# Kernel tuning notes

Hardware: AMD Instinct MI355X
Metric: run time of the kernel (lower is better)

## Reference

```python
import jax, jax.numpy as jnp
import numpy as np

BSZ, SEQ, D_IN = 256, 512, 1
STATE, D_OUT, KX = 512, 512, 5


def setup_inputs() -> dict:
    key = jax.random.key(0)
    k1, k2, k3, k4, k5, k6 = jax.random.split(key, 6)
    inputs = jax.random.normal(k1, (BSZ, SEQ, D_IN), dtype=jnp.float32)
    # diagonal transition, kept stable in (0, 0.99)
    A = jax.random.uniform(k2, (STATE,), dtype=jnp.float32, minval=0.0, maxval=0.99)
    B = jax.random.normal(k3, (D_IN, STATE), dtype=jnp.float32) * 0.05
    C = jax.random.normal(k4, (STATE, D_OUT), dtype=jnp.float32) * 0.05
    M = jax.random.normal(k5, (D_OUT, D_IN, KX), dtype=jnp.float32) * 0.05
    h0 = jax.random.normal(k6, (STATE,), dtype=jnp.float32)
    return {"inputs": inputs, "A": A, "B": B, "C": C, "M": M, "h0": h0}


def reference(inputs, A, B, C, M, h0):
    """LDS forward: h_t = A*h_{t-1} + x_t @ B; y_t = h_t @ C + sum_i M[:,:,i] x_{t-1-i}.
    inputs: [B, T, 1] -> out: [B, T, D_OUT]
    """
    bsz, T, _ = inputs.shape
    h_init = jnp.broadcast_to(h0, (bsz, h0.shape[0]))  # reset_state: h = h0 per batch row

    xs = jnp.swapaxes(inputs, 0, 1)  # [T, B, 1]

    def step(h, x_t):
        h = h * A + x_t @ B  # [B, STATE]
        return h, h

    _, hs = jax.lax.scan(step, h_init, xs)  # hs: [T, B, STATE]
    lds_out = jnp.einsum('tbs,so->bto', hs, C)  # [B, T, D_OUT]

    # AR ring buffer: at step t it holds x_{t-1}..x_{t-kx} (zeros before t=0),
    # tap i multiplies M[:,:,i]. With d_in==1 this is a delayed causal conv.
    x = inputs[:, :, 0]  # [B, T]
    kx = M.shape[-1]
    shifted = jnp.stack(
        [jnp.pad(x, ((0, 0), (i + 1, 0)))[:, :T] for i in range(kx)], axis=-1
    )  # [B, T, kx]; entry i is x_{t-1-i}
    ar_out = jnp.einsum('btk,ok->bto', shifted, M[:, 0, :])  # [B, T, D_OUT]

    return lds_out + ar_out
```

## Files before the change

kernel.cpp:

```cpp
#include <hip/hip_runtime.h>


typedef __attribute__((ext_vector_type(8))) short short8v;
typedef __attribute__((ext_vector_type(4))) float float4v;

#define NB 16
#define SIG(e) ((e) + ((e) >> 3))
#define AWI(j) ((((j) % 6) + 6) % 6)

static __device__ __forceinline__ unsigned short f2bf(float f) {
    union { float f; unsigned int u; } x; x.f = f;
    unsigned int r = x.u + 0x7fffu + ((x.u >> 16) & 1u);
    return (unsigned short)(r >> 16);
}

__global__ __launch_bounds__(256) void k_prep(const float* __restrict__ A,
                                              const float* __restrict__ B,
                                              const float* __restrict__ h0,
                                              const float* __restrict__ C,
                                              const float* __restrict__ M,
                                              const float* __restrict__ x,
                                              unsigned short* __restrict__ KT,
                                              float* __restrict__ G,
                                              short8v* __restrict__ XS) {
    __shared__ float PBL[512][4];
    __shared__ float PHL[512][4];
    __shared__ float red[4][64][8];
    __shared__ unsigned short xs[512];
    const int tid = threadIdx.x;

    if (blockIdx.x < 1024) {
        const int d0 = (blockIdx.x & 127) * 4;
        const int oc = blockIdx.x >> 7;

        #pragma unroll
        for (int q = 0; q < 2; ++q) {
            int ss = tid + q * 256;
            float a = A[ss];
            float r = 1.0f, base = a;
            #pragma unroll
            for (int bit = 0; bit < 9; ++bit) {
                if (d0 & (1 << bit)) r *= base;
                base *= base;
            }
            float bs = B[ss], hs = h0[ss];
            #pragma unroll
            for (int j = 0; j < 4; ++j) {
                PBL[ss][j] = r * bs;
                PHL[ss][j] = r * a * hs;
                r *= a;
            }
        }
        __syncthreads();

        const int lane = tid & 63;
        const int sc   = tid >> 6;
        const int o    = oc * 64 + lane;
        float kt[4] = {0.f, 0.f, 0.f, 0.f};
        float gg[4] = {0.f, 0.f, 0.f, 0.f};
        for (int si = 0; si < 128; si += 8) {
            float c8[8];
            #pragma unroll
            for (int u = 0; u < 8; ++u)
                c8[u] = C[(sc * 128 + si + u) * 512 + o];
            #pragma unroll
            for (int u = 0; u < 8; ++u) {
                int s = sc * 128 + si + u;
                #pragma unroll
                for (int j = 0; j < 4; ++j) {
                    kt[j] = fmaf(PBL[s][j], c8[u], kt[j]);
                    gg[j] = fmaf(PHL[s][j], c8[u], gg[j]);
                }
            }
        }
        #pragma unroll
        for (int j = 0; j < 4; ++j) {
            red[sc][lane][j]     = kt[j];
            red[sc][lane][j + 4] = gg[j];
        }
        __syncthreads();
        if (sc == 0) {
            #pragma unroll
            for (int j = 0; j < 4; ++j) {
                float v  = red[0][lane][j] + red[1][lane][j]
                         + red[2][lane][j] + red[3][lane][j];
                float gv = red[0][lane][j+4] + red[1][lane][j+4]
                         + red[2][lane][j+4] + red[3][lane][j+4];
                int d = d0 + j;
                if (d >= 1 && d <= 5) v += M[o * 5 + (d - 1)];
                KT[o * 512 + d] = f2bf(v);
                G[d * 512 + o]  = gv;
            }
        }
    } else {
        const int b = blockIdx.x - 1024;
        #pragma unroll
        for (int q = 0; q < 2; ++q) {
            int i = tid * 2 + q;
            xs[i] = f2bf(x[b * 512 + 511 - i]);
        }
        __syncthreads();
        short8v* dst = XS + (size_t)b * 1216;
        for (int s2 = tid; s2 < 1216; s2 += 256) {
            if (s2 % 9 == 8 || s2 > 1150) dst[s2] = (short8v)(short)0;
        }
        #pragma unroll
        for (int q = 0; q < 4; ++q) {
            int e = tid * 4 + q;
            short8v v;
            #pragma unroll
            for (int jj = 0; jj < 8; ++jj) {
                int i = e + jj;
                v[jj] = (i < 512) ? (short)xs[i] : (short)0;
            }
            dst[SIG(e)] = v;
        }
    }
}

__global__ __launch_bounds__(256, 2) void k_main(const short8v* __restrict__ XS,
                                                 const unsigned short* __restrict__ KT,
                                                 const float* __restrict__ G,
                                                 float* __restrict__ out) {
    __shared__ short8v xbuf[2][1216];

    const int bo0 = blockIdx.x * 32;
    const int bt0 = blockIdx.y * 256;
    const int b0  = blockIdx.z * NB;
    const int tid = threadIdx.x;
    const int lane = tid & 63;
    const int wv   = tid >> 6;
    const int t0w  = bt0 + wv * 64;
    const int lrow = lane & 15;
    const int g    = lane >> 4;

    {
        const short8v* src = XS + (size_t)b0 * 1216;
        for (int c = wv; c < 19; c += 4)
            __builtin_amdgcn_global_load_lds(
                (const __attribute__((address_space(1))) void*)(src + c * 64 + lane),
                (__attribute__((address_space(3))) void*)(&xbuf[0][c * 64]),
                16, 0, 0);
    }

    short8v bfr[2][16];
    #pragma unroll
    for (int ni = 0; ni < 2; ++ni) {
        const unsigned short* bp = KT + (bo0 + ni * 16 + lrow) * 512 + g * 8;
        #pragma unroll
        for (int ks = 0; ks < 16; ++ks)
            bfr[ni][ks] = *(const short8v*)(bp + ks * 32);
    }

    float4v gacc[4][2];
    #pragma unroll
    for (int mi = 0; mi < 4; ++mi)
        #pragma unroll
        for (int ni = 0; ni < 2; ++ni)
            gacc[mi][ni] = *(const float4v*)(G + (t0w + mi * 16 + lrow) * 512
                                               + bo0 + ni * 16 + g * 4);

    asm volatile("s_waitcnt vmcnt(0)" ::: "memory");
    __builtin_amdgcn_s_barrier();

    const int E0 = 511 - t0w - lrow + g * 8;

    int p = 0;
    for (int bi = 0; bi < NB; ++bi) {
        const int b = b0 + bi;

        if (bi + 1 < NB) {
            const short8v* src = XS + (size_t)(b + 1) * 1216;
            short8v* dstb = xbuf[p ^ 1];
            for (int c = wv; c < 19; c += 4)
                __builtin_amdgcn_global_load_lds(
                    (const __attribute__((address_space(1))) void*)(src + c * 64 + lane),
                    (__attribute__((address_space(3))) void*)(dstb + c * 64),
                    16, 0, 0);
        }

        const short8v* xo = xbuf[p];

        float4v acc[4][2];
        #pragma unroll
        for (int mi = 0; mi < 4; ++mi)
            #pragma unroll
            for (int ni = 0; ni < 2; ++ni)
                acc[mi][ni] = (float4v)(0.0f);

        short8v aw[6];
        #pragma unroll
        for (int j = -3; j <= 0; ++j)
            aw[AWI(j)] = xo[SIG(E0 + 16 * j)];

        __builtin_amdgcn_s_setprio(1);
        #pragma unroll
        for (int ks = 0; ks < 16; ++ks) {
            acc[3][0] = __builtin_amdgcn_mfma_f32_16x16x32_bf16(
                bfr[0][ks], aw[AWI(2 * ks - 3)], acc[3][0], 0, 0, 0);
            acc[3][1] = __builtin_amdgcn_mfma_f32_16x16x32_bf16(
                bfr[1][ks], aw[AWI(2 * ks - 3)], acc[3][1], 0, 0, 0);
            acc[2][0] = __builtin_amdgcn_mfma_f32_16x16x32_bf16(
                bfr[0][ks], aw[AWI(2 * ks - 2)], acc[2][0], 0, 0, 0);
            acc[2][1] = __builtin_amdgcn_mfma_f32_16x16x32_bf16(
                bfr[1][ks], aw[AWI(2 * ks - 2)], acc[2][1], 0, 0, 0);
            if (ks < 15) {
                aw[AWI(2 * ks + 1)] = xo[SIG(E0 + 16 * (2 * ks + 1))];
                aw[AWI(2 * ks + 2)] = xo[SIG(E0 + 16 * (2 * ks + 2))];
            }
            acc[1][0] = __builtin_amdgcn_mfma_f32_16x16x32_bf16(
                bfr[0][ks], aw[AWI(2 * ks - 1)], acc[1][0], 0, 0, 0);
            acc[1][1] = __builtin_amdgcn_mfma_f32_16x16x32_bf16(
                bfr[1][ks], aw[AWI(2 * ks - 1)], acc[1][1], 0, 0, 0);
            acc[0][0] = __builtin_amdgcn_mfma_f32_16x16x32_bf16(
                bfr[0][ks], aw[AWI(2 * ks)], acc[0][0], 0, 0, 0);
            acc[0][1] = __builtin_amdgcn_mfma_f32_16x16x32_bf16(
                bfr[1][ks], aw[AWI(2 * ks)], acc[0][1], 0, 0, 0);
        }
        __builtin_amdgcn_s_setprio(0);

        float* op = out + (size_t)b * 262144;
        #pragma unroll
        for (int mi = 0; mi < 4; ++mi) {
            const int t = t0w + mi * 16 + lrow;
            float* rp = op + t * 512 + bo0 + g * 4;
            *(float4v*)(rp)      = acc[mi][0] + gacc[mi][0];
            *(float4v*)(rp + 16) = acc[mi][1] + gacc[mi][1];
        }

        if (bi + 1 < NB) {
            asm volatile("s_waitcnt vmcnt(8)" ::: "memory");
            __builtin_amdgcn_s_barrier();
            p ^= 1;
        }
    }
}

extern "C" void kernel_launch(void* const* d_in, const int* in_sizes, int n_in,
                              void* d_out, int out_size, void* d_ws, size_t ws_size,
                              hipStream_t stream) {
    const float* x  = (const float*)d_in[0];
    const float* A  = (const float*)d_in[1];
    const float* B  = (const float*)d_in[2];
    const float* C  = (const float*)d_in[3];
    const float* M  = (const float*)d_in[4];
    const float* h0 = (const float*)d_in[5];
    float* out = (float*)d_out;

    char* ws = (char*)d_ws;
    unsigned short* KT = (unsigned short*)ws;
    float*          G  = (float*)(ws + (1u << 19));
    short8v*        XS = (short8v*)(ws + (1u << 19) + (1u << 20));

    k_prep<<<1280, 256, 0, stream>>>(A, B, h0, C, M, x, KT, G, XS);
    k_main<<<dim3(16, 2, 16), 256, 0, stream>>>(XS, KT, G, out);
}
```

Before: 87.09 us.

## Load sliding input windows directly from global memory instead of staging in LDS

Removes the double-buffered LDS staging of the per-batch Toeplitz input octets, along with the padded swizzle layout and its barriers. Each lane now reads its A-operand windows straight from a dense global buffer through registers, with an 8-deep register ring and prefetch of the next batch's window during the epilogue. The G bias is folded in as the initial accumulator value. This drops LDS traffic and block-wide synchronization, but relies on cache hits for the redundant global reads and exposes global load latency inside the MFMA loop.

```diff
diff --git a/kernel.cpp b/kernel.cpp
--- a/kernel.cpp
+++ b/kernel.cpp
@@ -5,8 +5,6 @@
 typedef __attribute__((ext_vector_type(4))) float float4v;
 
 #define NB 16
-#define SIG(e) ((e) + ((e) >> 3))
-#define AWI(j) ((((j) % 6) + 6) % 6)
 
 static __device__ __forceinline__ unsigned short f2bf(float f) {
     union { float f; unsigned int u; } x; x.f = f;
@@ -22,7 +20,7 @@
                                               const float* __restrict__ x,
                                               unsigned short* __restrict__ KT,
                                               float* __restrict__ G,
-                                              short8v* __restrict__ XS) {
+                                              short8v* __restrict__ XOCT) {
     __shared__ float PBL[512][4];
     __shared__ float PHL[512][4];
     __shared__ float red[4][64][8];
@@ -100,10 +98,7 @@
             xs[i] = f2bf(x[b * 512 + 511 - i]);
         }
         __syncthreads();
-        short8v* dst = XS + (size_t)b * 1216;
-        for (int s2 = tid; s2 < 1216; s2 += 256) {
-            if (s2 % 9 == 8 || s2 > 1150) dst[s2] = (short8v)(short)0;
-        }
+        short8v* dst = XOCT + (size_t)b * 1024;
         #pragma unroll
         for (int q = 0; q < 4; ++q) {
             int e = tid * 4 + q;
@@ -113,36 +108,25 @@
                 int i = e + jj;
                 v[jj] = (i < 512) ? (short)xs[i] : (short)0;
             }
-            dst[SIG(e)] = v;
+            dst[e] = v;
         }
     }
 }
 
-__global__ __launch_bounds__(256, 2) void k_main(const short8v* __restrict__ XS,
+__global__ __launch_bounds__(256, 2) void k_main(const short8v* __restrict__ XOCT,
                                                  const unsigned short* __restrict__ KT,
                                                  const float* __restrict__ G,
                                                  float* __restrict__ out) {
-    __shared__ short8v xbuf[2][1216];
-
     const int bo0 = blockIdx.x * 32;
     const int bt0 = blockIdx.y * 256;
     const int b0  = blockIdx.z * NB;
-    const int tid = threadIdx.x;
+    const int tid  = threadIdx.x;
     const int lane = tid & 63;
     const int wv   = tid >> 6;
     const int t0w  = bt0 + wv * 64;
     const int lrow = lane & 15;
     const int g    = lane >> 4;
 
-    {
-        const short8v* src = XS + (size_t)b0 * 1216;
-        for (int c = wv; c < 19; c += 4)
-            __builtin_amdgcn_global_load_lds(
-                (const __attribute__((address_space(1))) void*)(src + c * 64 + lane),
-                (__attribute__((address_space(3))) void*)(&xbuf[0][c * 64]),
-                16, 0, 0);
-    }
-
     short8v bfr[2][16];
     #pragma unroll
     for (int ni = 0; ni < 2; ++ni) {
@@ -151,7 +135,6 @@
         for (int ks = 0; ks < 16; ++ks)
             bfr[ni][ks] = *(const short8v*)(bp + ks * 32);
     }
-
     float4v gacc[4][2];
     #pragma unroll
     for (int mi = 0; mi < 4; ++mi)
@@ -160,78 +143,62 @@
             gacc[mi][ni] = *(const float4v*)(G + (t0w + mi * 16 + lrow) * 512
                                                + bo0 + ni * 16 + g * 4);
 
-    asm volatile("s_waitcnt vmcnt(0)" ::: "memory");
-    __builtin_amdgcn_s_barrier();
-
-    const int E0 = 511 - t0w - lrow + g * 8;
-
-    int p = 0;
+    const int E0 = 511 - t0w - lrow + 8 * g;
+    const short8v* xw = XOCT + (size_t)b0 * 1024 + E0;
+
+    short8v aw[8];
+    #pragma unroll
+    for (int j = -3; j <= 4; ++j)
+        aw[j & 7] = xw[16 * j];
+
     for (int bi = 0; bi < NB; ++bi) {
-        const int b = b0 + bi;
-
-        if (bi + 1 < NB) {
-            const short8v* src = XS + (size_t)(b + 1) * 1216;
-            short8v* dstb = xbuf[p ^ 1];
-            for (int c = wv; c < 19; c += 4)
-                __builtin_amdgcn_global_load_lds(
-                    (const __attribute__((address_space(1))) void*)(src + c * 64 + lane),
-                    (__attribute__((address_space(3))) void*)(dstb + c * 64),
-                    16, 0, 0);
-        }
-
-        const short8v* xo = xbuf[p];
-
         float4v acc[4][2];
         #pragma unroll
         for (int mi = 0; mi < 4; ++mi)
             #pragma unroll
             for (int ni = 0; ni < 2; ++ni)
-                acc[mi][ni] = (float4v)(0.0f);
-
-        short8v aw[6];
-        #pragma unroll
-        for (int j = -3; j <= 0; ++j)
-            aw[AWI(j)] = xo[SIG(E0 + 16 * j)];
+                acc[mi][ni] = gacc[mi][ni];
 
         __builtin_amdgcn_s_setprio(1);
         #pragma unroll
         for (int ks = 0; ks < 16; ++ks) {
             acc[3][0] = __builtin_amdgcn_mfma_f32_16x16x32_bf16(
-                bfr[0][ks], aw[AWI(2 * ks - 3)], acc[3][0], 0, 0, 0);
+                bfr[0][ks], aw[(2 * ks - 3) & 7], acc[3][0], 0, 0, 0);
             acc[3][1] = __builtin_amdgcn_mfma_f32_16x16x32_bf16(
-                bfr[1][ks], aw[AWI(2 * ks - 3)], acc[3][1], 0, 0, 0);
+                bfr[1][ks], aw[(2 * ks - 3) & 7], acc[3][1], 0, 0, 0);
             acc[2][0] = __builtin_amdgcn_mfma_f32_16x16x32_bf16(
-                bfr[0][ks], aw[AWI(2 * ks - 2)], acc[2][0], 0, 0, 0);
+                bfr[0][ks], aw[(2 * ks - 2) & 7], acc[2][0], 0, 0, 0);
             acc[2][1] = __builtin_amdgcn_mfma_f32_16x16x32_bf16(
-                bfr[1][ks], aw[AWI(2 * ks - 2)], acc[2][1], 0, 0, 0);
-            if (ks < 15) {
-                aw[AWI(2 * ks + 1)] = xo[SIG(E0 + 16 * (2 * ks + 1))];
-                aw[AWI(2 * ks + 2)] = xo[SIG(E0 + 16 * (2 * ks + 2))];
+                bfr[1][ks], aw[(2 * ks - 2) & 7], acc[2][1], 0, 0, 0);
+            if (ks <= 12) {
+                aw[(2 * ks + 5) & 7] = xw[16 * (2 * ks + 5)];
+                aw[(2 * ks + 6) & 7] = xw[16 * (2 * ks + 6)];
             }
             acc[1][0] = __builtin_amdgcn_mfma_f32_16x16x32_bf16(
-                bfr[0][ks], aw[AWI(2 * ks - 1)], acc[1][0], 0, 0, 0);
+                bfr[0][ks], aw[(2 * ks - 1) & 7], acc[1][0], 0, 0, 0);
             acc[1][1] = __builtin_amdgcn_mfma_f32_16x16x32_bf16(
-                bfr[1][ks], aw[AWI(2 * ks - 1)], acc[1][1], 0, 0, 0);
+                bfr[1][ks], aw[(2 * ks - 1) & 7], acc[1][1], 0, 0, 0);
             acc[0][0] = __builtin_amdgcn_mfma_f32_16x16x32_bf16(
-                bfr[0][ks], aw[AWI(2 * ks)], acc[0][0], 0, 0, 0);
+                bfr[0][ks], aw[(2 * ks) & 7], acc[0][0], 0, 0, 0);
             acc[0][1] = __builtin_amdgcn_mfma_f32_16x16x32_bf16(
-                bfr[1][ks], aw[AWI(2 * ks)], acc[0][1], 0, 0, 0);
+                bfr[1][ks], aw[(2 * ks) & 7], acc[0][1], 0, 0, 0);
         }
         __builtin_amdgcn_s_setprio(0);
 
-        float* op = out + (size_t)b * 262144;
+        if (bi + 1 < NB) {
+            xw += 1024;
+            #pragma unroll
+            for (int j = -3; j <= 4; ++j)
+                aw[j & 7] = xw[16 * j];
+        }
+
+        float* op = out + (size_t)(b0 + bi) * 262144;
         #pragma unroll
         for (int mi = 0; mi < 4; ++mi) {
             const int t = t0w + mi * 16 + lrow;
             float* rp = op + t * 512 + bo0 + g * 4;
-            *(float4v*)(rp)      = acc[mi][0] + gacc[mi][0];
-            *(float4v*)(rp + 16) = acc[mi][1] + gacc[mi][1];
-        }
-
-        if (bi + 1 < NB) {
-            asm volatile("s_waitcnt vmcnt(8)" ::: "memory");
-            __builtin_amdgcn_s_barrier();
-            p ^= 1;
+            *(float4v*)(rp)      = acc[mi][0];
+            *(float4v*)(rp + 16) = acc[mi][1];
         }
     }
 }
@@ -248,10 +215,10 @@
     float* out = (float*)d_out;
 
     char* ws = (char*)d_ws;
-    unsigned short* KT = (unsigned short*)ws;
-    float*          G  = (float*)(ws + (1u << 19));
-    short8v*        XS = (short8v*)(ws + (1u << 19) + (1u << 20));
-
-    k_prep<<<1280, 256, 0, stream>>>(A, B, h0, C, M, x, KT, G, XS);
-    k_main<<<dim3(16, 2, 16), 256, 0, stream>>>(XS, KT, G, out);
-}
+    unsigned short* KT   = (unsigned short*)ws;
+    float*          G    = (float*)(ws + (1u << 19));
+    short8v*        XOCT = (short8v*)(ws + (1u << 19) + (1u << 20));
+
+    k_prep<<<1280, 256, 0, stream>>>(A, B, h0, C, M, x, KT, G, XOCT);
+    k_main<<<dim3(16, 2, 16), 256, 0, stream>>>(XOCT, KT, G, out);
+}
```

Measured after the change: 115.1 us. +32.1%, slower.
